# Kernel optimization log

Hardware: AMD Instinct MI355X
Metric: run time of the kernel (lower is better)

The kernel has to match this reference:

```python
import jax, jax.numpy as jnp
import numpy as np

THRESHOLD = 0.4


def _pair_feat(xs, xd):
    # pair_mode='both': [src, dst, |src-dst|, src*dst] along feature axis
    return jnp.concatenate([xs, xd, jnp.abs(xs - xd), xs * xd], axis=-1)


def _mlp(pf, W1, b1, W2, b2):
    h = jax.nn.relu(pf @ W1 + b1)
    return (h @ W2 + b2)[..., 0]


def setup_inputs() -> dict:
    key = jax.random.key(0)
    k1, k2, k3, k4, k5 = jax.random.split(key, 5)
    N, F, E, H = 1024, 64, 65536, 32
    x = jax.random.normal(k1, (N, F), dtype=jnp.float32)
    edge_index = jax.random.randint(k2, (2, E), 0, N, dtype=jnp.int64)
    edge_index_global = jax.random.randint(k3, (2, E), 0, N, dtype=jnp.int64)
    W1 = jax.random.normal(k4, (4 * F, H), dtype=jnp.float32) * (1.0 / np.sqrt(4 * F))
    b1 = jnp.zeros((H,), dtype=jnp.float32)
    W2 = jax.random.normal(k5, (H, 1), dtype=jnp.float32) * (1.0 / np.sqrt(H))
    b2 = jnp.zeros((1,), dtype=jnp.float32)
    return {"x": x, "edge_index": edge_index, "edge_index_global": edge_index_global,
            "W1": W1, "b1": b1, "W2": W2, "b2": b2}


def reference(x, edge_index, edge_index_global, W1, b1, W2, b2):
    # ---- sparse edge branch ----
    xs = x[edge_index[0]]            # [E, F]
    xd = x[edge_index[1]]            # [E, F]
    pf = _pair_feat(xs, xd)          # [E, 4F]
    edge_logits = _mlp(pf, W1, b1, W2, b2)        # [E]
    edge_probs = jax.nn.sigmoid(edge_logits)      # [E]
    edge_actions = (edge_probs > THRESHOLD).astype(x.dtype)  # [E]
    # (new_edge_index / raw_edge_index in the original are data-dependent
    #  boolean selections of edge columns; the mask is edge_actions==1.)

    # ---- dense all-pairs branch (train=True) ----
    N, F = x.shape
    xi = jnp.broadcast_to(x[:, None, :], (N, N, F))  # src of pair (i,j)
    xj = jnp.broadcast_to(x[None, :, :], (N, N, F))  # dst of pair (i,j)
    pf_all = _pair_feat(xi, xj)                      # [N, N, 4F] -- dominant intermediate
    logits_all = _mlp(pf_all, W1, b1, W2, b2)        # [N, N]
    P = jax.nn.sigmoid(logits_all)                   # [N, N]

    return edge_probs, edge_actions, P
```

## Files before the change

kernel.cpp:

```cpp
#include <hip/hip_runtime.h>
#include <hip/hip_bf16.h>
#include <math.h>

#define NN 1024
#define FD 64
#define EE 65536
#define HD 32

typedef __attribute__((ext_vector_type(8))) short short8;
typedef __attribute__((ext_vector_type(4))) float floatx4;

__device__ __forceinline__ float sigmoid_f(float z) {
  return 1.0f / (1.0f + expf(-z));
}
__device__ __forceinline__ float sigmoid_fast(float z) {
  return 1.0f / (1.0f + __expf(-z));
}

__device__ __forceinline__ unsigned pack_bf16_trunc(float hi, float lo) {
  unsigned a = __builtin_bit_cast(unsigned, hi);
  unsigned b = __builtin_bit_cast(unsigned, lo);
  return __builtin_amdgcn_perm(a, b, 0x07060302u);
}

__device__ __forceinline__ short8 pack8(const float* v) {
  union { unsigned u[4]; short8 s; } p;
#pragma unroll
  for (int t = 0; t < 4; ++t) p.u[t] = pack_bf16_trunc(v[2 * t + 1], v[2 * t]);
  return p.s;
}

struct Frag3 { short8 a0, a1, a2; };

__device__ __forceinline__ Frag3 split_pack(const float* v) {
  float r[8], r2[8];
#pragma unroll
  for (int t = 0; t < 8; ++t) {
    const unsigned uv = __builtin_bit_cast(unsigned, v[t]);
    const float f0 = __builtin_bit_cast(float, uv & 0xFFFF0000u);
    const float rr = v[t] - f0;
    const unsigned ur = __builtin_bit_cast(unsigned, rr);
    const float f1 = __builtin_bit_cast(float, ur & 0xFFFF0000u);
    r[t] = rr;
    r2[t] = rr - f1;
  }
  Frag3 f;
  f.a0 = pack8(v);
  f.a1 = pack8(r);
  f.a2 = pack8(r2);
  return f;
}

__global__ __launch_bounds__(256) void pre_kernel3(
    const float* __restrict__ x, const float* __restrict__ W1,
    const float* __restrict__ b1, float* __restrict__ pre,
    short* __restrict__ Wt0, short* __restrict__ Wt1, short* __restrict__ Wt2) {
  const int blk = blockIdx.x;
  const int t = threadIdx.x;
  if (blk < 256) {
    const int node = blk * 4 + (t >> 6);
    const int which = (t >> 5) & 1;
    const int h = t & 31;
    const float* xr = x + node * FD;
    const float* wp = W1 + which * FD * HD + h;
    float a0 = which ? 0.0f : b1[h], a1 = 0.0f, a2 = 0.0f, a3 = 0.0f;
#pragma unroll
    for (int f = 0; f < FD; f += 4) {
      a0 = fmaf(xr[f + 0], wp[(f + 0) * HD], a0);
      a1 = fmaf(xr[f + 1], wp[(f + 1) * HD], a1);
      a2 = fmaf(xr[f + 2], wp[(f + 2) * HD], a2);
      a3 = fmaf(xr[f + 3], wp[(f + 3) * HD], a3);
    }
    pre[which * (NN * HD) + node * HD + h] = (a0 + a1) + (a2 + a3);
  } else {
    for (int idx = t; idx < 32 * 128; idx += 256) {
      const int h = idx >> 7;
      const int k = idx & 127;
      const int f = k & 63;
      const int b = 2 + (k >> 6);
      const float v = W1[(b * FD + f) * HD + h];
      const unsigned uv = __builtin_bit_cast(unsigned, v);
      const unsigned u0 = uv & 0xFFFF0000u;
      const float f0 = __builtin_bit_cast(float, u0);
      const float r = v - f0;
      const unsigned u1 = __builtin_bit_cast(unsigned, r) & 0xFFFF0000u;
      const float f1 = __builtin_bit_cast(float, u1);
      const float r2 = r - f1;
      const unsigned u2 = __builtin_bit_cast(unsigned, r2) & 0xFFFF0000u;
      Wt0[idx] = (short)(u0 >> 16);
      Wt1[idx] = (short)(u1 >> 16);
      Wt2[idx] = (short)(u2 >> 16);
    }
  }
}

__device__ __forceinline__ void edge_chunk(
    const float* feat, const short* __restrict__ Wt0,
    const short* __restrict__ Wt1, const short* __restrict__ Wt2,
    int c, int q, int kc, floatx4& acc0, floatx4& acc1) {
  const Frag3 B = split_pack(feat);
  const int off0 = c * 128 + kc * 32 + q * 8;
  const int off1 = (16 + c) * 128 + kc * 32 + q * 8;
  const short8 A00 = *(const short8*)(Wt0 + off0);
  const short8 A01 = *(const short8*)(Wt1 + off0);
  const short8 A02 = *(const short8*)(Wt2 + off0);
  const short8 A10 = *(const short8*)(Wt0 + off1);
  const short8 A11 = *(const short8*)(Wt1 + off1);
  const short8 A12 = *(const short8*)(Wt2 + off1);
  acc0 = __builtin_amdgcn_mfma_f32_16x16x32_bf16(A00, B.a0, acc0, 0, 0, 0);
  acc0 = __builtin_amdgcn_mfma_f32_16x16x32_bf16(A01, B.a0, acc0, 0, 0, 0);
  acc0 = __builtin_amdgcn_mfma_f32_16x16x32_bf16(A02, B.a0, acc0, 0, 0, 0);
  acc0 = __builtin_amdgcn_mfma_f32_16x16x32_bf16(A00, B.a1, acc0, 0, 0, 0);
  acc0 = __builtin_amdgcn_mfma_f32_16x16x32_bf16(A01, B.a1, acc0, 0, 0, 0);
  acc0 = __builtin_amdgcn_mfma_f32_16x16x32_bf16(A00, B.a2, acc0, 0, 0, 0);
  acc1 = __builtin_amdgcn_mfma_f32_16x16x32_bf16(A10, B.a0, acc1, 0, 0, 0);
  acc1 = __builtin_amdgcn_mfma_f32_16x16x32_bf16(A11, B.a0, acc1, 0, 0, 0);
  acc1 = __builtin_amdgcn_mfma_f32_16x16x32_bf16(A12, B.a0, acc1, 0, 0, 0);
  acc1 = __builtin_amdgcn_mfma_f32_16x16x32_bf16(A10, B.a1, acc1, 0, 0, 0);
  acc1 = __builtin_amdgcn_mfma_f32_16x16x32_bf16(A11, B.a1, acc1, 0, 0, 0);
  acc1 = __builtin_amdgcn_mfma_f32_16x16x32_bf16(A10, B.a2, acc1, 0, 0, 0);
}

__global__ __launch_bounds__(256, 3) void edge_mfma_kernel(
    const float* __restrict__ x, const int* __restrict__ eidx,
    const float* __restrict__ pre, const short* __restrict__ Wt0,
    const short* __restrict__ Wt1, const short* __restrict__ Wt2,
    const float* __restrict__ W2, const float* __restrict__ b2,
    float* __restrict__ out) {
  const int lane = threadIdx.x & 63;
  const int q = lane >> 4;
  const int c = lane & 15;
  const int e0 = (blockIdx.x * 4 + (threadIdx.x >> 6)) * 16;

  const bool is64 = (eidx[1] == 0) && (eidx[3] == 0) && (eidx[5] == 0);
  int s_c, d_c;
  if (is64) {
    s_c = eidx[2 * (e0 + c)];
    d_c = eidx[2 * (EE + e0 + c)];
  } else {
    s_c = eidx[e0 + c];
    d_c = eidx[EE + e0 + c];
  }
  const float* xs = x + (size_t)s_c * FD;
  const float* xd = x + (size_t)d_c * FD;

  floatx4 acc0, acc1;
  {
    const floatx4 psA = *(const floatx4*)(pre + s_c * HD + q * 4);
    const floatx4 psB = *(const floatx4*)(pre + s_c * HD + 16 + q * 4);
    const floatx4 pdA = *(const floatx4*)(pre + NN * HD + d_c * HD + q * 4);
    const floatx4 pdB = *(const floatx4*)(pre + NN * HD + d_c * HD + 16 + q * 4);
#pragma unroll
    for (int r = 0; r < 4; ++r) {
      acc0[r] = psA[r] + pdA[r];
      acc1[r] = psB[r] + pdB[r];
    }
  }

  {
    const floatx4 s0 = *(const floatx4*)(xs + q * 8);
    const floatx4 s1 = *(const floatx4*)(xs + q * 8 + 4);
    const floatx4 d0 = *(const floatx4*)(xd + q * 8);
    const floatx4 d1 = *(const floatx4*)(xd + q * 8 + 4);
    float ad[8], pr[8];
#pragma unroll
    for (int t = 0; t < 4; ++t) {
      ad[t] = fabsf(s0[t] - d0[t]);     pr[t] = s0[t] * d0[t];
      ad[4 + t] = fabsf(s1[t] - d1[t]); pr[4 + t] = s1[t] * d1[t];
    }
    edge_chunk(ad, Wt0, Wt1, Wt2, c, q, 0, acc0, acc1);
    edge_chunk(pr, Wt0, Wt1, Wt2, c, q, 2, acc0, acc1);
  }
  {
    const floatx4 s0 = *(const floatx4*)(xs + 32 + q * 8);
    const floatx4 s1 = *(const floatx4*)(xs + 32 + q * 8 + 4);
    const floatx4 d0 = *(const floatx4*)(xd + 32 + q * 8);
    const floatx4 d1 = *(const floatx4*)(xd + 32 + q * 8 + 4);
    float ad[8], pr[8];
#pragma unroll
    for (int t = 0; t < 4; ++t) {
      ad[t] = fabsf(s0[t] - d0[t]);     pr[t] = s0[t] * d0[t];
      ad[4 + t] = fabsf(s1[t] - d1[t]); pr[4 + t] = s1[t] * d1[t];
    }
    edge_chunk(ad, Wt0, Wt1, Wt2, c, q, 1, acc0, acc1);
    edge_chunk(pr, Wt0, Wt1, Wt2, c, q, 3, acc0, acc1);
  }

  const floatx4 w2A = *(const floatx4*)(W2 + q * 4);
  const floatx4 w2B = *(const floatx4*)(W2 + 16 + q * 4);
  float tv = 0.0f;
#pragma unroll
  for (int r = 0; r < 4; ++r) {
    tv = fmaf(fmaxf(acc0[r], 0.0f), w2A[r], tv);
    tv = fmaf(fmaxf(acc1[r], 0.0f), w2B[r], tv);
  }
  tv += __shfl_xor(tv, 16);
  tv += __shfl_xor(tv, 32);
  if (lane < 16) {
    const int e = e0 + lane;
    const float z = tv + b2[0];
    out[e] = sigmoid_f(z);
    out[EE + e] = (z > -0.40546510810816444f) ? 1.0f : 0.0f;
  }
}

__global__ __launch_bounds__(256, 4) void dense_mfma_kernel(
    const float* __restrict__ x, const float* __restrict__ pre,
    const short* __restrict__ Wt0, const float* __restrict__ W2,
    const float* __restrict__ b2, float* __restrict__ outP) {
  const int lane = threadIdx.x & 63;
  const int w = threadIdx.x >> 6;
  const int q = lane >> 4;
  const int c = lane & 15;
  const int j0 = blockIdx.x * 64 + w * 16;
  const int i0 = blockIdx.y * 16;

  short8 Af[2][4];
#pragma unroll
  for (int n = 0; n < 2; ++n)
#pragma unroll
    for (int s = 0; s < 4; ++s)
      Af[n][s] = *(const short8*)(Wt0 + (n * 16 + c) * 128 + s * 32 + q * 8);

  const float* xj = x + (size_t)(j0 + c) * FD;
  float jA[8], jB[8];
#pragma unroll
  for (int t = 0; t < 4; ++t) {
    jA[t] = xj[q * 8 + t];      jA[4 + t] = xj[q * 8 + 4 + t];
    jB[t] = xj[32 + q * 8 + t]; jB[4 + t] = xj[32 + q * 8 + 4 + t];
  }

  const floatx4 pdA = *(const floatx4*)(pre + NN * HD + (j0 + c) * HD + q * 4);
  const floatx4 pdB = *(const floatx4*)(pre + NN * HD + (j0 + c) * HD + 16 + q * 4);
  const floatx4 w2A = *(const floatx4*)(W2 + q * 4);
  const floatx4 w2B = *(const floatx4*)(W2 + 16 + q * 4);
  const float b2v = b2[0];

  for (int i = i0; i < i0 + 16; ++i) {
    const float* xi = x + (size_t)i * FD;
    const floatx4 psA = *(const floatx4*)(pre + i * HD + q * 4);
    const floatx4 psB = *(const floatx4*)(pre + i * HD + 16 + q * 4);
    floatx4 acc0, acc1;
#pragma unroll
    for (int r = 0; r < 4; ++r) {
      acc0[r] = psA[r] + pdA[r];
      acc1[r] = psB[r] + pdB[r];
    }
    {
      const floatx4 i0v = *(const floatx4*)(xi + q * 8);
      const floatx4 i1v = *(const floatx4*)(xi + q * 8 + 4);
      float ad[8], pr[8];
#pragma unroll
      for (int t = 0; t < 4; ++t) {
        ad[t] = fabsf(i0v[t] - jA[t]);         pr[t] = i0v[t] * jA[t];
        ad[4 + t] = fabsf(i1v[t] - jA[4 + t]); pr[4 + t] = i1v[t] * jA[4 + t];
      }
      const short8 fad = pack8(ad);
      const short8 fpr = pack8(pr);
      acc0 = __builtin_amdgcn_mfma_f32_16x16x32_bf16(Af[0][0], fad, acc0, 0, 0, 0);
      acc1 = __builtin_amdgcn_mfma_f32_16x16x32_bf16(Af[1][0], fad, acc1, 0, 0, 0);
      acc0 = __builtin_amdgcn_mfma_f32_16x16x32_bf16(Af[0][2], fpr, acc0, 0, 0, 0);
      acc1 = __builtin_amdgcn_mfma_f32_16x16x32_bf16(Af[1][2], fpr, acc1, 0, 0, 0);
    }
    {
      const floatx4 i0v = *(const floatx4*)(xi + 32 + q * 8);
      const floatx4 i1v = *(const floatx4*)(xi + 32 + q * 8 + 4);
      float ad[8], pr[8];
#pragma unroll
      for (int t = 0; t < 4; ++t) {
        ad[t] = fabsf(i0v[t] - jB[t]);         pr[t] = i0v[t] * jB[t];
        ad[4 + t] = fabsf(i1v[t] - jB[4 + t]); pr[4 + t] = i1v[t] * jB[4 + t];
      }
      const short8 fad = pack8(ad);
      const short8 fpr = pack8(pr);
      acc0 = __builtin_amdgcn_mfma_f32_16x16x32_bf16(Af[0][1], fad, acc0, 0, 0, 0);
      acc1 = __builtin_amdgcn_mfma_f32_16x16x32_bf16(Af[1][1], fad, acc1, 0, 0, 0);
      acc0 = __builtin_amdgcn_mfma_f32_16x16x32_bf16(Af[0][3], fpr, acc0, 0, 0, 0);
      acc1 = __builtin_amdgcn_mfma_f32_16x16x32_bf16(Af[1][3], fpr, acc1, 0, 0, 0);
    }
    float tv = 0.0f;
#pragma unroll
    for (int r = 0; r < 4; ++r) {
      tv = fmaf(fmaxf(acc0[r], 0.0f), w2A[r], tv);
      tv = fmaf(fmaxf(acc1[r], 0.0f), w2B[r], tv);
    }
    tv += __shfl_xor(tv, 16);
    tv += __shfl_xor(tv, 32);
    if (lane < 16) {
      outP[(size_t)i * NN + j0 + lane] = sigmoid_fast(tv + b2v);
    }
  }
}

__device__ __forceinline__ float pair_logit_full(
    const float* __restrict__ xs, const float* __restrict__ xd,
    const float* __restrict__ W1, const float* __restrict__ b1,
    const float* __restrict__ W2, const float b2v) {
  float acc[HD];
#pragma unroll
  for (int h = 0; h < HD; ++h) acc[h] = b1[h];
#pragma unroll 1
  for (int f = 0; f < FD; ++f) {
    const float a = xs[f], b = xd[f];
    const float ad = fabsf(a - b), pr = a * b;
#pragma unroll
    for (int h = 0; h < HD; ++h) {
      float t0 = fmaf(a, W1[f * HD + h], acc[h]);
      t0 = fmaf(b, W1[(FD + f) * HD + h], t0);
      t0 = fmaf(ad, W1[(2 * FD + f) * HD + h], t0);
      acc[h] = fmaf(pr, W1[(3 * FD + f) * HD + h], t0);
    }
  }
  float z = b2v;
#pragma unroll
  for (int h = 0; h < HD; ++h) z = fmaf(fmaxf(acc[h], 0.0f), W2[h], z);
  return z;
}

__global__ __launch_bounds__(256) void edge_kernel_fb(
    const float* __restrict__ x, const int* __restrict__ eidx,
    const float* __restrict__ W1, const float* __restrict__ b1,
    const float* __restrict__ W2, const float* __restrict__ b2,
    float* __restrict__ out) {
  const int e = blockIdx.x * 256 + threadIdx.x;
  const bool is64 = (eidx[1] == 0) && (eidx[3] == 0) && (eidx[5] == 0);
  int s, d;
  if (is64) { s = eidx[2 * e]; d = eidx[2 * (EE + e)]; }
  else { s = eidx[e]; d = eidx[EE + e]; }
  const float z = pair_logit_full(x + (size_t)s * FD, x + (size_t)d * FD,
                                  W1, b1, W2, b2[0]);
  const float p = sigmoid_f(z);
  out[e] = p;
  out[EE + e] = (p > 0.4f) ? 1.0f : 0.0f;
}

__global__ __launch_bounds__(256) void dense_full_fb(
    const float* __restrict__ x, const float* __restrict__ W1,
    const float* __restrict__ b1, const float* __restrict__ W2,
    const float* __restrict__ b2, float* __restrict__ outP) {
  const int j = blockIdx.x * 64 + threadIdx.x % 64;
  const int i = blockIdx.y * 4 + threadIdx.x / 64;
  const float z = pair_logit_full(x + (size_t)i * FD, x + (size_t)j * FD,
                                  W1, b1, W2, b2[0]);
  outP[(size_t)i * NN + j] = sigmoid_f(z);
}

extern "C" void kernel_launch(void* const* d_in, const int* in_sizes, int n_in,
                              void* d_out, int out_size, void* d_ws, size_t ws_size,
                              hipStream_t stream) {
  const float* x  = (const float*)d_in[0];
  const int*  ei  = (const int*)d_in[1];
  const float* W1 = (const float*)d_in[3];
  const float* b1 = (const float*)d_in[4];
  const float* W2 = (const float*)d_in[5];
  const float* b2 = (const float*)d_in[6];
  float* out  = (float*)d_out;
  float* outP = out + 2 * EE;

  const size_t pre_bytes = (size_t)2 * NN * HD * sizeof(float);
  const size_t wt_elems = 32 * 128;
  const size_t need = pre_bytes + 3 * wt_elems * sizeof(short);
  if (ws_size >= need) {
    float* pre = (float*)d_ws;
    short* Wt0 = (short*)((char*)d_ws + pre_bytes);
    short* Wt1 = Wt0 + wt_elems;
    short* Wt2 = Wt1 + wt_elems;
    pre_kernel3<<<257, 256, 0, stream>>>(x, W1, b1, pre, Wt0, Wt1, Wt2);
    edge_mfma_kernel<<<1024, 256, 0, stream>>>(x, ei, pre, Wt0, Wt1, Wt2,
                                               W2, b2, out);
    dense_mfma_kernel<<<dim3(16, 64), 256, 0, stream>>>(x, pre, Wt0, W2, b2,
                                                        outP);
  } else {
    edge_kernel_fb<<<EE / 256, 256, 0, stream>>>(x, ei, W1, b1, W2, b2, out);
    dense_full_fb<<<dim3(NN / 64, NN / 4), 256, 0, stream>>>(
        x, W1, b1, W2, b2, outP);
  }
}
```

Measured before the change: 112.3 us.

## Exploit symmetry of abs/product pair features to compute only upper-triangle tiles

The |xi-xj| and xi*xj feature terms are symmetric in i and j, so the MFMA contribution from those terms is shared between P[i,j] and P[j,i]. Warps whose column tile lies below the row tile now exit early, and off-diagonal warps reuse the accumulated MFMA result to produce the transposed entry by adding the swapped src/dst precomputed terms. This roughly halves the matrix-core work. In exchange, half the warps sit idle, which leaves work unevenly spread across blocks. The transposed writes are strided (column-wise) and uncoalesced, and launch bounds were relaxed to 2 blocks per CU.

```diff
diff --git a/kernel.cpp b/kernel.cpp
--- a/kernel.cpp
+++ b/kernel.cpp
@@ -204,7 +204,7 @@
   }
 }
 
-__global__ __launch_bounds__(256, 4) void dense_mfma_kernel(
+__global__ __launch_bounds__(256, 2) void dense_mfma_sym_kernel(
     const float* __restrict__ x, const float* __restrict__ pre,
     const short* __restrict__ Wt0, const float* __restrict__ W2,
     const float* __restrict__ b2, float* __restrict__ outP) {
@@ -214,6 +214,8 @@
   const int c = lane & 15;
   const int j0 = blockIdx.x * 64 + w * 16;
   const int i0 = blockIdx.y * 16;
+  if (j0 < i0) return;
+  const bool offdiag = (j0 > i0);
 
   short8 Af[2][4];
 #pragma unroll
@@ -230,22 +232,21 @@
     jB[t] = xj[32 + q * 8 + t]; jB[4 + t] = xj[32 + q * 8 + 4 + t];
   }
 
-  const floatx4 pdA = *(const floatx4*)(pre + NN * HD + (j0 + c) * HD + q * 4);
-  const floatx4 pdB = *(const floatx4*)(pre + NN * HD + (j0 + c) * HD + 16 + q * 4);
+  const floatx4 psA_j = *(const floatx4*)(pre + (j0 + c) * HD + q * 4);
+  const floatx4 psB_j = *(const floatx4*)(pre + (j0 + c) * HD + 16 + q * 4);
+  const floatx4 pdA_j = *(const floatx4*)(pre + NN * HD + (j0 + c) * HD + q * 4);
+  const floatx4 pdB_j = *(const floatx4*)(pre + NN * HD + (j0 + c) * HD + 16 + q * 4);
   const floatx4 w2A = *(const floatx4*)(W2 + q * 4);
   const floatx4 w2B = *(const floatx4*)(W2 + 16 + q * 4);
   const float b2v = b2[0];
 
   for (int i = i0; i < i0 + 16; ++i) {
     const float* xi = x + (size_t)i * FD;
-    const floatx4 psA = *(const floatx4*)(pre + i * HD + q * 4);
-    const floatx4 psB = *(const floatx4*)(pre + i * HD + 16 + q * 4);
-    floatx4 acc0, acc1;
-#pragma unroll
-    for (int r = 0; r < 4; ++r) {
-      acc0[r] = psA[r] + pdA[r];
-      acc1[r] = psB[r] + pdB[r];
-    }
+    const floatx4 psA_i = *(const floatx4*)(pre + i * HD + q * 4);
+    const floatx4 psB_i = *(const floatx4*)(pre + i * HD + 16 + q * 4);
+    floatx4 acc0 = {0.0f, 0.0f, 0.0f, 0.0f};
+    floatx4 acc1 = {0.0f, 0.0f, 0.0f, 0.0f};
+
     {
       const floatx4 i0v = *(const floatx4*)(xi + q * 8);
       const floatx4 i1v = *(const floatx4*)(xi + q * 8 + 4);
@@ -278,16 +279,33 @@
       acc0 = __builtin_amdgcn_mfma_f32_16x16x32_bf16(Af[0][3], fpr, acc0, 0, 0, 0);
       acc1 = __builtin_amdgcn_mfma_f32_16x16x32_bf16(Af[1][3], fpr, acc1, 0, 0, 0);
     }
+
     float tv = 0.0f;
 #pragma unroll
     for (int r = 0; r < 4; ++r) {
-      tv = fmaf(fmaxf(acc0[r], 0.0f), w2A[r], tv);
-      tv = fmaf(fmaxf(acc1[r], 0.0f), w2B[r], tv);
+      tv = fmaf(fmaxf(acc0[r] + psA_i[r] + pdA_j[r], 0.0f), w2A[r], tv);
+      tv = fmaf(fmaxf(acc1[r] + psB_i[r] + pdB_j[r], 0.0f), w2B[r], tv);
     }
     tv += __shfl_xor(tv, 16);
     tv += __shfl_xor(tv, 32);
     if (lane < 16) {
       outP[(size_t)i * NN + j0 + lane] = sigmoid_fast(tv + b2v);
+    }
+
+    if (offdiag) {
+      const floatx4 pdA_i = *(const floatx4*)(pre + NN * HD + i * HD + q * 4);
+      const floatx4 pdB_i = *(const floatx4*)(pre + NN * HD + i * HD + 16 + q * 4);
+      float tm = 0.0f;
+#pragma unroll
+      for (int r = 0; r < 4; ++r) {
+        tm = fmaf(fmaxf(acc0[r] + psA_j[r] + pdA_i[r], 0.0f), w2A[r], tm);
+        tm = fmaf(fmaxf(acc1[r] + psB_j[r] + pdB_i[r], 0.0f), w2B[r], tm);
+      }
+      tm += __shfl_xor(tm, 16);
+      tm += __shfl_xor(tm, 32);
+      if (q == 1) {
+        outP[(size_t)(j0 + c) * NN + i] = sigmoid_fast(tm + b2v);
+      }
     }
   }
 }
@@ -368,8 +386,8 @@
     pre_kernel3<<<257, 256, 0, stream>>>(x, W1, b1, pre, Wt0, Wt1, Wt2);
     edge_mfma_kernel<<<1024, 256, 0, stream>>>(x, ei, pre, Wt0, Wt1, Wt2,
                                                W2, b2, out);
-    dense_mfma_kernel<<<dim3(16, 64), 256, 0, stream>>>(x, pre, Wt0, W2, b2,
-                                                        outP);
+    dense_mfma_sym_kernel<<<dim3(16, 64), 256, 0, stream>>>(x, pre, Wt0, W2,
+                                                            b2, outP);
   } else {
     edge_kernel_fb<<<EE / 256, 256, 0, stream>>>(x, ei, W1, b1, W2, b2, out);
     dense_full_fb<<<dim3(NN / 64, NN / 4), 256, 0, stream>>>(
```

After: 118.4 us. 5.4% more time.
